# Performance work log

Measured on AMD Instinct MI355X. Metric: run time of the kernel, lower is better.

Reference implementation:

```python
import jax, jax.numpy as jnp
import numpy as np

K = 16
EPS = 1e-5
SLOPE = 0.01  # nn.LeakyReLU default


def _bn(x, g, b):
    # BatchNorm1d in training mode applied to [N, C, k] in torch == normalize
    # per-channel over (N, k) axes of [N, k, C] here. Biased variance (ddof=0).
    m = x.mean(axis=(0, 1))
    v = x.var(axis=(0, 1))
    return (x - m) * jax.lax.rsqrt(v + EPS) * g + b


def _lrelu(x):
    return jnp.where(x >= 0, x, SLOPE * x)


def setup_inputs() -> dict:
    key = jax.random.key(0)
    ks = jax.random.split(key, 24)
    N, CIN, COUT = 8192, 256, 256
    s = 0.05
    inp = {
        "fea_i": jax.random.normal(ks[0], (N, CIN), jnp.float32),
        "fea_last": jax.random.normal(ks[1], (N, CIN), jnp.float32),
        "xyz_i": jax.random.uniform(ks[2], (N, 3), jnp.float32),
        "xyz_last": jax.random.uniform(ks[3], (N, 3), jnp.float32),
        "t_i": jnp.float32(2.0),
        "t_last": jnp.float32(1.0),
        # lin_p: Linear(4,64) -> BN(64) -> LeakyReLU -> Linear(64,COUT)
        "wp1": jax.random.normal(ks[4], (4, 64), jnp.float32) * s,
        "bp1": jnp.zeros((64,), jnp.float32),
        "gp": jnp.ones((64,), jnp.float32),
        "bp": jnp.zeros((64,), jnp.float32),
        "wp2": jax.random.normal(ks[5], (64, COUT), jnp.float32) * s,
        "bp2": jnp.zeros((COUT,), jnp.float32),
        # lin_q / lin_k / lin_v
        "wq": jax.random.normal(ks[6], (CIN, COUT), jnp.float32) * s,
        "bq": jnp.zeros((COUT,), jnp.float32),
        "wk": jax.random.normal(ks[7], (CIN, COUT), jnp.float32) * s,
        "bk": jnp.zeros((COUT,), jnp.float32),
        "wv": jax.random.normal(ks[8], (CIN, COUT), jnp.float32) * s,
        "bv": jnp.zeros((COUT,), jnp.float32),
        # lin_w: BN -> LeakyReLU -> Linear(COUT,COUT) -> BN -> LeakyReLU
        "gw1": jnp.ones((COUT,), jnp.float32),
        "bw1": jnp.zeros((COUT,), jnp.float32),
        "ww": jax.random.normal(ks[9], (COUT, COUT), jnp.float32) * s,
        "bw": jnp.zeros((COUT,), jnp.float32),
        "gw2": jnp.ones((COUT,), jnp.float32),
        "bw2": jnp.zeros((COUT,), jnp.float32),
    }
    return inp


def reference(fea_i, fea_last, xyz_i, xyz_last, t_i, t_last,
              wp1, bp1, gp, bp, wp2, bp2,
              wq, bq, wk, bk, wv, bv,
              gw1, bw1, ww, bw, gw2, bw2):
    # k-NN: for each query point in xyz_last, K nearest points in xyz_i
    d2 = (jnp.sum(xyz_last * xyz_last, -1)[:, None]
          + jnp.sum(xyz_i * xyz_i, -1)[None, :]
          - 2.0 * xyz_last @ xyz_i.T)              # [N, N]
    idx = jax.lax.top_k(-d2, K)[1]                 # [N, K] neighbor idx into xyz_i

    fi = fea_i[idx]                                # [N, K, CIN]
    xi = xyz_i[idx]                                # [N, K, 3]
    # pe = xyzt_i - xyzt_last ; the gathered "last" side is the query point itself
    pe = jnp.concatenate([xi - xyz_last[:, None, :],
                          (t_i - t_last) * jnp.ones_like(xi[..., :1])], axis=-1)  # [N,K,4]
    pe = pe @ wp1 + bp1
    pe = _lrelu(_bn(pe, gp, bp))
    pe = pe @ wp2 + bp2                            # [N, K, COUT]

    q = fea_last @ wq + bq                         # [N, COUT], broadcast over K
    w = q[:, None, :] - (fi @ wk + bk) + pe        # [N, K, COUT]
    w = _lrelu(_bn(w, gw1, bw1))
    w = w @ ww + bw
    w = _lrelu(_bn(w, gw2, bw2))
    w = jax.nn.softmax(w, axis=1)                  # softmax over K neighbors

    v = fi @ wv + bv + pe                          # [N, K, COUT]
    return jnp.sum(w * v, axis=1)                  # [N, COUT]
```

## Files before the change

### kernel.cpp

```cpp
#include <hip/hip_runtime.h>
#include <hip/hip_bf16.h>
#include <math.h>

#define N     8192
#define KNN   16
#define NK    (N*KNN)
#define C     256
#define CH    64
#define EPS   1e-5f
#define SLOPE 0.01f
#define LISTMAX 512

typedef __hip_bfloat16 bf16;
typedef short bfrag __attribute__((ext_vector_type(8)));
typedef float ffrag __attribute__((ext_vector_type(4)));

__device__ __forceinline__ float b2f(bf16 x){ return __bfloat162float(x); }
__device__ __forceinline__ bf16  f2b(float x){ return __float2bfloat16(x); }
__device__ __forceinline__ float b2fu(unsigned short s){
    return __uint_as_float(((unsigned)s) << 16);
}
__device__ __forceinline__ unsigned short f2bu(float x){
    union { bf16 h; unsigned short s; } u; u.h = f2b(x); return u.s;
}

union BF8 { unsigned short s[8]; uint4 u; };

template<typename T> __device__ __forceinline__ float ldv(const void* p, int i);
template<> __device__ __forceinline__ float ldv<float>(const void* p, int i){
    return ((const float*)p)[i];
}
template<> __device__ __forceinline__ float ldv<bf16>(const void* p, int i){
    return __bfloat162float(((const bf16*)p)[i]);
}
__device__ __forceinline__ bool is_f32(const void* ti){
    return ((const unsigned short*)ti)[0] == 0;
}

template<typename T>
__device__ __forceinline__ void stage8(const void* src, size_t off,
                                       unsigned short* dst){
    if (sizeof(T) == 4){
        const float4* s = (const float4*)((const float*)src + off);
        float4 a = s[0], b = s[1];
        BF8 o;
        o.s[0]=f2bu(a.x); o.s[1]=f2bu(a.y); o.s[2]=f2bu(a.z); o.s[3]=f2bu(a.w);
        o.s[4]=f2bu(b.x); o.s[5]=f2bu(b.y); o.s[6]=f2bu(b.z); o.s[7]=f2bu(b.w);
        *(uint4*)dst = o.u;
    } else {
        *(uint4*)dst = *(const uint4*)((const unsigned short*)src + off);
    }
}

__device__ __forceinline__ int mbcnt64(unsigned long long b){
    return __builtin_amdgcn_mbcnt_hi((unsigned)(b>>32),
           __builtin_amdgcn_mbcnt_lo((unsigned)b, 0));
}
__device__ __forceinline__ unsigned d2key(float d2){
    unsigned u = __float_as_uint(d2);
    return u ^ (((unsigned)(((int)u) >> 31)) | 0x80000000u);
}

__device__ __align__(256) int    g_idx[NK];
__device__ __align__(256) float  g_S[4096];
__device__ __align__(256) float  g_Rep[4*64*256];
__device__ __align__(256) float  g_M2[2048*9];
__device__ __align__(256) float4 g_pts[N];
__device__ __align__(256) float4 g_qlast[N];
__device__ __align__(256) int    g_cellCnt[4096];
__device__ __align__(256) int    g_cellStart[4100];
__device__ __align__(256) int    g_cellCur[4096];
__device__ __align__(256) float4 g_spts[N];
__device__ __align__(256) int    g_sidx[N];
__device__ __align__(256) unsigned short g_qT [C*C];
__device__ __align__(256) unsigned short g_kT [C*C];
__device__ __align__(256) unsigned short g_vT [C*C];
__device__ __align__(256) unsigned short g_wwT[C*C];
__device__ __align__(256) unsigned short g_p2T[C*CH];
__device__ __align__(256) unsigned short g_q  [N*C];
__device__ __align__(256) unsigned short g_fkb[N*C];
__device__ __align__(256) unsigned short g_fvb[N*C];
__device__ __align__(256) bf16   g_w1[NK*C];
__device__ __align__(256) bf16   g_vv[NK*C];
__device__ __align__(256) bf16   g_w2[NK*C];

__device__ __forceinline__ int cell_of(float4 c){
    int cx = (int)(c.x*16.f); cx = cx<0?0:(cx>15?15:cx);
    int cy = (int)(c.y*16.f); cy = cy<0?0:(cy>15?15:cy);
    int cz = (int)(c.z*16.f); cz = cz<0?0:(cz>15?15:cz);
    return (cz<<8) | (cy<<4) | cx;
}

__global__ __launch_bounds__(256) void kprepall(const void* xyz_i,
        const void* xyz_last,
        const void* wq, const void* wk, const void* wv, const void* ww,
        const void* wp2, const void* ti_){
#pragma clang fp contract(off)
    const int b = blockIdx.x, tid = threadIdx.x;
    const bool f = is_f32(ti_);
    if (b < 64){
        int i = b*256 + tid;
        #pragma unroll
        for (int k = 0; k < 4; k++) g_Rep[i*4 + k] = 0.f;
        if (b < 16) g_S[i] = 0.f;
        else if (b < 32) g_cellCnt[(b-16)*256 + tid] = 0;
    } else if (b < 96){
        int p = (b-64)*256 + tid;
        float x = f ? ldv<float>(xyz_i, p*3+0) : ldv<bf16>(xyz_i, p*3+0);
        float y = f ? ldv<float>(xyz_i, p*3+1) : ldv<bf16>(xyz_i, p*3+1);
        float z = f ? ldv<float>(xyz_i, p*3+2) : ldv<bf16>(xyz_i, p*3+2);
        g_pts[p] = make_float4(x, y, z, (x*x + y*y) + z*z);
    } else if (b < 128){
        int p = (b-96)*256 + tid;
        float x = f ? ldv<float>(xyz_last, p*3+0) : ldv<bf16>(xyz_last, p*3+0);
        float y = f ? ldv<float>(xyz_last, p*3+1) : ldv<bf16>(xyz_last, p*3+1);
        float z = f ? ldv<float>(xyz_last, p*3+2) : ldv<bf16>(xyz_last, p*3+2);
        g_qlast[p] = make_float4(x, y, z, 0.f);
    } else {
        const void* src; unsigned short* dst; int K; int i0;
        if      (b <  384){ src=wq;  dst=g_qT;  K=256; i0=(b- 128)*256; }
        else if (b <  640){ src=wk;  dst=g_kT;  K=256; i0=(b- 384)*256; }
        else if (b <  896){ src=wv;  dst=g_vT;  K=256; i0=(b- 640)*256; }
        else if (b < 1152){ src=ww;  dst=g_wwT; K=256; i0=(b- 896)*256; }
        else              { src=wp2; dst=g_p2T; K=64;  i0=(b-1152)*256; }
        int i = i0 + tid;
        int k = i >> 8, n = i & 255;
        float v = f ? ldv<float>(src, i) : ldv<bf16>(src, i);
        dst[n*K + k] = f2bu(v);
    }
}

__global__ __launch_bounds__(256) void khist(){
    int p = blockIdx.x*256 + threadIdx.x;
    atomicAdd(&g_cellCnt[cell_of(g_pts[p])], 1);
}
__global__ __launch_bounds__(256) void kscan(){
    __shared__ int sc[256];
    const int tid = threadIdx.x;
    int carry = 0;
    for (int ch = 0; ch < 16; ch++){
        int i = ch*256 + tid;
        int v = g_cellCnt[i];
        sc[tid] = v;
        __syncthreads();
        for (int s = 1; s < 256; s <<= 1){
            int t_ = (tid >= s) ? sc[tid - s] : 0;
            __syncthreads();
            sc[tid] += t_;
            __syncthreads();
        }
        int excl = carry + sc[tid] - v;
        g_cellStart[i] = excl;
        g_cellCur[i]   = excl;
        carry += sc[255];
        __syncthreads();
    }
    if (tid == 0) g_cellStart[4096] = carry;
}
__global__ __launch_bounds__(256) void kscatter(){
    int p = blockIdx.x*256 + threadIdx.x;
    float4 c = g_pts[p];
    int pos = atomicAdd(&g_cellCur[cell_of(c)], 1);
    g_spts[pos] = c;
    g_sidx[pos] = p;
}

template<int D>
__device__ unsigned sel16(float qx, float qy, float qz, float sq, int lane){
#pragma clang fp contract(off)
    unsigned kk[D];
    #pragma unroll
    for (int i = 0; i < D; i++) kk[i] = 0xFFFFFFFFu;
    for (int t = 0; t < N/64; t++){
        float4 c = g_pts[t*64 + lane];
        float dot = (qx*c.x + qy*c.y) + qz*c.z;
        float d2  = (sq + c.w) - 2.0f*dot;
        unsigned u = d2key(d2);
        #pragma unroll
        for (int j = D-1; j > 0; --j){
            unsigned hi = (kk[j-1] > u) ? kk[j-1] : u;
            kk[j] = (kk[j] < hi) ? kk[j] : hi;
        }
        kk[0] = (kk[0] < u) ? kk[0] : u;
    }
    unsigned v16 = 0;
    for (int it = 0; it < 16; ++it){
        unsigned m = kk[0];
        #pragma unroll
        for (int s = 1; s < 64; s <<= 1){
            unsigned o = (unsigned)__shfl_xor((int)m, s, 64);
            m = (m < o) ? m : o;
        }
        unsigned long long ball = __ballot(kk[0] == m);
        int w = __ffsll(ball) - 1;
        if (lane == w){
            #pragma unroll
            for (int j = 0; j < D-1; j++) kk[j] = kk[j+1];
            kk[D-1] = 0xFFFFFFFFu;
        }
        v16 = m;
    }
    return v16;
}

__device__ int2 scan16(float qx, float qy, float qz, float sq, unsigned v16,
                       int lane, int* sure, int* tie){
#pragma clang fp contract(off)
    int nsure = 0, ntie = 0;
    for (int t = 0; t < N/64; t++){
        const int p = t*64 + lane;
        float4 c = g_pts[p];
        float dot = (qx*c.x + qy*c.y) + qz*c.z;
        float d2  = (sq + c.w) - 2.0f*dot;
        unsigned u = d2key(d2);
        bool bs = (u < v16), bt = (u == v16);
        unsigned long long Bs = __ballot(bs);
        unsigned long long Bt = __ballot(bt);
        if (bs){
            int pos = nsure + mbcnt64(Bs);
            if (pos < 16) sure[pos] = p;
        }
        if (bt){
            int pos = ntie + mbcnt64(Bt);
            if (pos < 16) tie[pos] = p;
        }
        nsure += (int)__popcll(Bs);
        ntie  += (int)__popcll(Bt);
    }
    return make_int2(nsure, ntie);
}

template<typename T>
__device__ void kknn_body(const void* xyz_last, int* sureL, int* tieL,
                          int* listL, float* momL){
#pragma clang fp contract(off)
    const int lane  = threadIdx.x & 63;
    const int wslot = threadIdx.x >> 6;
    const int q     = (blockIdx.x*256 + threadIdx.x) >> 6;
    const float qx = ldv<T>(xyz_last, q*3+0);
    const float qy = ldv<T>(xyz_last, q*3+1);
    const float qz = ldv<T>(xyz_last, q*3+2);
    const float sq = (qx*qx + qy*qy) + qz*qz;
    int* sure = &sureL[wslot*16];
    int* tie  = &tieL [wslot*16];
    int* list = &listL[wslot*LISTMAX];

    int cqx = (int)(qx*16.f); cqx = cqx<0?0:(cqx>15?15:cqx);
    int cqy = (int)(qy*16.f); cqy = cqy<0?0:(cqy>15?15:cqy);
    int cqz = (int)(qz*16.f); cqz = cqz<0?0:(cqz>15?15:cqz);

    int cnt0 = 0, cnt1 = 0, cs0 = 0, cs1 = 0;
    #pragma unroll
    for (int h = 0; h < 2; h++){
        int idx = lane*2 + h;
        if (idx < 125){
            int iz = idx/25, r = idx - iz*25, iy = r/5, ix = r - iy*5;
            int cx = cqx+ix-2, cy = cqy+iy-2, cz = cqz+iz-2;
            if ((unsigned)cx < 16u && (unsigned)cy < 16u && (unsigned)cz < 16u){
                int cell = (cz<<8) | (cy<<4) | cx;
                int s = g_cellStart[cell], e = g_cellStart[cell+1];
                if (h == 0){ cs0 = s; cnt0 = e - s; }
                else       { cs1 = s; cnt1 = e - s; }
            }
        }
    }
    int tot = cnt0 + cnt1;
    int incl = tot;
    #pragma unroll
    for (int s = 1; s < 64; s <<= 1){
        int u = __shfl_up(incl, s, 64);
        if (lane >= s) incl += u;
    }
    const int Tn = __shfl(incl, 63, 64);
    int base = incl - tot;
    bool full = (Tn > LISTMAX) || (Tn < 16);
    unsigned v16 = 0;
    int nsure = 0, ntie = 0;
    if (!full){
        for (int i = 0; i < cnt0; i++) list[base+i] = cs0 + i;
        for (int i = 0; i < cnt1; i++) list[base+cnt0+i] = cs1 + i;
        unsigned kk[4] = {~0u,~0u,~0u,~0u};
        int chunks = (Tn + 63) >> 6;
        for (int t = 0; t < chunks; t++){
            int li = t*64 + lane;
            unsigned u = 0xFFFFFFFFu;
            if (li < Tn){
                float4 c = g_spts[list[li]];
                float dot = (qx*c.x + qy*c.y) + qz*c.z;
                u = d2key((sq + c.w) - 2.0f*dot);
            }
            #pragma unroll
            for (int j = 3; j > 0; --j){
                unsigned hi = (kk[j-1] > u) ? kk[j-1] : u;
                kk[j] = (kk[j] < hi) ? kk[j] : hi;
            }
            kk[0] = (kk[0] < u) ? kk[0] : u;
        }
        for (int it = 0; it < 16; ++it){
            unsigned m = kk[0];
            #pragma unroll
            for (int s = 1; s < 64; s <<= 1){
                unsigned o = (unsigned)__shfl_xor((int)m, s, 64);
                m = (m < o) ? m : o;
            }
            unsigned long long ball = __ballot(kk[0] == m);
            int w = __ffsll(ball) - 1;
            if (lane == w){
                kk[0]=kk[1]; kk[1]=kk[2]; kk[2]=kk[3]; kk[3]=0xFFFFFFFFu;
            }
            v16 = m;
        }
        const float h_ = 0.0625f;
        float dmin = 1e30f;
        if (cqx-2 > 0)  dmin = fminf(dmin, qx - (float)(cqx-2)*h_);
        if (cqx+3 < 16) dmin = fminf(dmin, (float)(cqx+3)*h_ - qx);
        if (cqy-2 > 0)  dmin = fminf(dmin, qy - (float)(cqy-2)*h_);
        if (cqy+3 < 16) dmin = fminf(dmin, (float)(cqy+3)*h_ - qy);
        if (cqz-2 > 0)  dmin = fminf(dmin, qz - (float)(cqz-2)*h_);
        if (cqz+3 < 16) dmin = fminf(dmin, (float)(cqz+3)*h_ - qz);
        unsigned ub = d2key(dmin*dmin);
        if (!(v16 < ub)) full = true;
    }
    if (!full){
        int chunks = (Tn + 63) >> 6;
        for (int t = 0; t < chunks; t++){
            int li = t*64 + lane;
            unsigned u = 0xFFFFFFFFu; int oi = 0;
            if (li < Tn){
                int pos = list[li];
                float4 c = g_spts[pos];
                oi = g_sidx[pos];
                float dot = (qx*c.x + qy*c.y) + qz*c.z;
                u = d2key((sq + c.w) - 2.0f*dot);
            }
            bool bs = (li < Tn) && (u < v16);
            bool bt = (li < Tn) && (u == v16);
            unsigned long long Bs = __ballot(bs);
            unsigned long long Bt = __ballot(bt);
            if (bs){
                int pos2 = nsure + mbcnt64(Bs);
                if (pos2 < 16) sure[pos2] = oi;
            }
            if (bt){
                int pos2 = ntie + mbcnt64(Bt);
                if (pos2 < 16) tie[pos2] = oi;
            }
            nsure += (int)__popcll(Bs);
            ntie  += (int)__popcll(Bt);
        }
        if (nsure > 16 || (ntie > 16 && nsure < 16)) full = true;
    }
    const bool gridok = !full;
    if (full){
        v16 = sel16<16>(qx, qy, qz, sq, lane);
        int2 c2 = scan16(qx, qy, qz, sq, v16, lane, sure, tie);
        nsure = c2.x; ntie = c2.y;
    }
    if (nsure > 16) nsure = 16;
    int vsel = 0;
    if (lane < 16 && lane < nsure) vsel = sure[lane];
    if (gridok){
        int tv = (lane < (ntie < 16 ? ntie : 16)) ? tie[lane] : 0x7FFFFFFF;
        #pragma unroll
        for (int k = 2; k <= 16; k <<= 1)
            #pragma unroll
            for (int j = k>>1; j > 0; j >>= 1){
                int o = __shfl_xor(tv, j, 64);
                bool asc = ((lane & k) == 0);
                bool low = ((lane & j) == 0);
                int mn = tv < o ? tv : o;
                int mx = tv < o ? o : tv;
                tv = (asc == low) ? mn : mx;
            }
        int tfrom = __shfl(tv, (lane - nsure) & 63, 64);
        if (lane < 16 && lane >= nsure) vsel = tfrom;
    } else {
        if (lane < 16 && lane >= nsure) vsel = tie[lane - nsure];
    }
    float dx = 0.f, dy = 0.f, dz = 0.f;
    if (lane < 16){
        if ((unsigned)vsel >= (unsigned)N) vsel = 0;
        g_idx[q*KNN + lane] = vsel;
        float4 c = g_pts[vsel];
        dx = c.x - qx; dy = c.y - qy; dz = c.z - qz;
    }
    float mm[9] = {dx, dy, dz, dx*dx, dx*dy, dx*dz, dy*dy, dy*dz, dz*dz};
    #pragma unroll
    for (int j = 0; j < 9; j++){
        #pragma unroll
        for (int s = 1; s < 16; s <<= 1)
            mm[j] += __shfl_xor(mm[j], s, 64);
    }
    if (lane == 0){
        #pragma unroll
        for (int j = 0; j < 9; j++) momL[wslot*9 + j] = mm[j];
    }
    __syncthreads();
    if (threadIdx.x < 9){
        int t = threadIdx.x;
        g_M2[blockIdx.x*9 + t] = momL[t] + momL[9+t] + momL[18+t] + momL[27+t];
    }
}
__global__ __launch_bounds__(256) void kknn(const void* xyz_last, const void* ti_){
    __shared__ int sureL[4*16];
    __shared__ int tieL [4*16];
    __shared__ int listL[4*LISTMAX];
    __shared__ float momL[4*9];
    if (is_f32(ti_)) kknn_body<float>(xyz_last, sureL, tieL, listL, momL);
    else             kknn_body<bf16 >(xyz_last, sureL, tieL, listL, momL);
}

template<typename T>
__device__ void kgemm3m_body(const void* A, const unsigned short* BT,
                             const void* bias, unsigned short* out,
                             unsigned short* Al, unsigned short* Bl){
    const int tid  = threadIdx.x;
    const int c0   = blockIdx.x*128, r0 = blockIdx.y*128;
    const int lane = tid & 63, wv = tid >> 6;
    const int m    = lane & 15, qd = lane >> 4;
    const int rw   = (wv >> 1)*64, cw = (wv & 1)*64;
    ffrag acc[4][4];
    #pragma unroll
    for (int i = 0; i < 4; i++)
        #pragma unroll
        for (int j = 0; j < 4; j++)
            #pragma unroll
            for (int r = 0; r < 4; r++) acc[i][j][r] = 0.f;
    const int arow = tid >> 2, ach = tid & 3;
    for (int kt = 0; kt < 8; ++kt){
        __syncthreads();
        #pragma unroll
        for (int p = 0; p < 2; ++p){
            int row = arow + p*64;
            stage8<T>(A, (size_t)(r0+row)*C + kt*32 + ach*8, &Al[row*40 + ach*8]);
            *(uint4*)&Bl[row*40 + ach*8] =
                *(const uint4*)&BT[(c0+row)*C + kt*32 + ach*8];
        }
        __syncthreads();
        bfrag af[4], bfr[4];
        #pragma unroll
        for (int i = 0; i < 4; i++)
            af[i] = *(const bfrag*)&Al[(rw + i*16 + m)*40 + qd*8];
        #pragma unroll
        for (int j = 0; j < 4; j++)
            bfr[j] = *(const bfrag*)&Bl[(cw + j*16 + m)*40 + qd*8];
        #pragma unroll
        for (int i = 0; i < 4; i++)
            #pragma unroll
            for (int j = 0; j < 4; j++)
                acc[i][j] = __builtin_amdgcn_mfma_f32_16x16x32_bf16(
                                af[i], bfr[j], acc[i][j], 0, 0, 0);
    }
    float b4[4];
    #pragma unroll
    for (int j = 0; j < 4; j++) b4[j] = ldv<T>(bias, c0 + cw + j*16 + m);
    #pragma unroll
    for (int i = 0; i < 4; i++){
        #pragma unroll
        for (int r = 0; r < 4; r++){
            int row = r0 + rw + i*16 + qd*4 + r;
            unsigned short* orow = &out[(size_t)row*C];
            #pragma unroll
            for (int j = 0; j < 4; j++)
                orow[c0 + cw + j*16 + m] = f2bu(acc[i][j][r] + b4[j]);
        }
    }
}
__global__ __launch_bounds__(256) void kgemm3m(const void* fea_i, const void* fea_last,
        const void* bq, const void* bk, const void* bv, const void* ti_){
    __shared__ unsigned short Al[128*40];
    __shared__ unsigned short Bl[128*40];
    const int which = blockIdx.z;
    const void* A = (which==0) ? fea_last : fea_i;
    const unsigned short* BT = (which==0) ? g_qT : (which==1) ? g_kT : g_vT;
    const void* bias = (which==0) ? bq : (which==1) ? bk : bv;
    unsigned short* out = (which==0) ? g_q : (which==1) ? g_fkb : g_fvb;
    if (is_f32(ti_)) kgemm3m_body<float>(A, BT, bias, out, Al, Bl);
    else             kgemm3m_body<bf16 >(A, BT, bias, out, Al, Bl);
}

template<typename T>
__device__ void kfinpe_body(const void* wp1, const void* bp1,
                            const void* gp, const void* bp_,
                            const void* t_i, const void* t_last,
                            float* mTot, float* wred){
    const int tid = threadIdx.x, lane = tid & 63, wv = tid >> 6;
    float p[9];
    #pragma unroll
    for (int j = 0; j < 9; j++) p[j] = 0.f;
    for (int i = tid; i < 2048; i += 256){
        const float* m = &g_M2[i*9];
        #pragma unroll
        for (int j = 0; j < 9; j++) p[j] += m[j];
    }
    #pragma unroll
    for (int j = 0; j < 9; j++){
        #pragma unroll
        for (int s = 1; s < 64; s <<= 1) p[j] += __shfl_xor(p[j], s, 64);
    }
    if (lane == 0){
        #pragma unroll
        for (int j = 0; j < 9; j++) wred[wv*9 + j] = p[j];
    }
    __syncthreads();
    if (tid < 9) mTot[tid] = wred[tid] + wred[9+tid] + wred[18+tid] + wred[27+tid];
    __syncthreads();
    if (tid >= 64) return;
    const int c = tid;
    float M[9];
    #pragma unroll
    for (int j = 0; j < 9; j++) M[j] = mTot[j];
    const float w0 = ldv<T>(wp1, c),     w1 = ldv<T>(wp1, 64+c);
    const float w2 = ldv<T>(wp1, 128+c), w3 = ldv<T>(wp1, 192+c);
    const float dt = ldv<T>(t_i, 0) - ldv<T>(t_last, 0);
    const float be = dt*w3 + ldv<T>(bp1, c);
    const float NKf = (float)NK;
    float lin  = w0*M[0] + w1*M[1] + w2*M[2];
    float quad = w0*w0*M[3] + w1*w1*M[6] + w2*w2*M[8]
               + 2.f*(w0*w1*M[4] + w0*w2*M[5] + w1*w2*M[7]);
    float mean = (lin + NKf*be) / NKf;
    float ev2  = (quad + 2.f*be*lin + NKf*be*be) / NKf;
    float var  = ev2 - mean*mean;
    float sc   = ldv<T>(gp, c) * rsqrtf(var + EPS);
    g_S[128+c] = sc;
    g_S[192+c] = ldv<T>(bp_, c) - mean*sc;
}
__global__ void kfinpe(const void* wp1, const void* bp1, const void* gp,
                       const void* bp_, const void* t_i, const void* t_last){
    __shared__ float mTot[9];
    __shared__ float wred[4*9];
    if (is_f32(t_i)) kfinpe_body<float>(wp1, bp1, gp, bp_, t_i, t_last, mTot, wred);
    else             kfinpe_body<bf16 >(wp1, bp1, gp, bp_, t_i, t_last, mTot, wred);
}

__global__ void kfinalize(int Cn, int outOff, const void* g, const void* b,
                          const void* ti_, int repA){
    int c = threadIdx.x;
    if (c >= Cn) return;
    float s = 0.f, ss = 0.f;
    for (int r = 0; r < 64; r++){
        s  += g_Rep[((repA  )*64 + r)*256 + c];
        ss += g_Rep[((repA+1)*64 + r)*256 + c];
    }
    bool f = is_f32(ti_);
    float mean = s / (float)NK;
    float var  = ss / (float)NK - mean*mean;
    float gv = f ? ldv<float>(g, c) : ldv<bf16>(g, c);
    float bv = f ? ldv<float>(b, c) : ldv<bf16>(b, c);
    float sc = gv * rsqrtf(var + EPS);
    g_S[outOff+c]    = sc;
    g_S[outOff+Cn+c] = bv - mean*sc;
}

#define PE_LDP 132
template<typename T>
__device__ void kpe2m_body(const void* wp1, const void* bp1, const void* bp2,
                           const void* t_i, const void* t_last,
                           unsigned short* Apel, unsigned short* Bpl,
                           float* peL, int* gl, float* s1w, float* s2w){
    const int tid  = threadIdx.x;
    const int lane = tid & 63, wv = tid >> 6;
    const int m    = lane & 15, qd = lane >> 4;
    const int rw   = (wv >> 2)*64, cw = (wv & 3)*64;
    const int r0   = blockIdx.x*128;
    if (tid < 128) gl[tid] = g_idx[r0 + tid];
    { int row = tid >> 1, half = tid & 1;
      #pragma unroll
      for (int e = 0; e < 4; e++)
          *(uint4*)&Bpl[row*72 + half*32 + e*8] =
              *(const uint4*)&g_p2T[row*CH + half*32 + e*8];
    }
    __syncthreads();
    { const int kp = lane;
      const float w0 = ldv<T>(wp1, kp),     w1 = ldv<T>(wp1, 64+kp);
      const float w2 = ldv<T>(wp1, 128+kp), w3 = ldv<T>(wp1, 192+kp);
      const float b0 = ldv<T>(bp1, kp);
      const float sc = g_S[128+kp], sh = g_S[128+64+kp];
      const float dt = ldv<T>(t_i, 0) - ldv<T>(t_last, 0);
      #pragma unroll 4
      for (int p = 0; p < 16; p++){
          int row = wv*16 + p;
          int R = r0 + row; int n = R >> 4; int g = gl[row];
          float4 cp = g_pts[g];
          float4 qp = g_qlast[n];
          float dx = cp.x - qp.x;
          float dy = cp.y - qp.y;
          float dz = cp.z - qp.z;
          float v = dx*w0 + dy*w1 + dz*w2 + dt*w3 + b0;
          v = v*sc + sh;
          v = (v >= 0.f) ? v : SLOPE*v;
          Apel[row*72 + kp] = f2bu(v);
      } }
    __syncthreads();
    ffrag acc[4][4];
    #pragma unroll
    for (int i = 0; i < 4; i++)
        #pragma unroll
        for (int j = 0; j < 4; j++)
            #pragma unroll
            for (int r = 0; r < 4; r++) acc[i][j][r] = 0.f;
    #pragma unroll
    for (int ks = 0; ks < 2; ++ks){
        bfrag af[4], bfr[4];
        #pragma unroll
        for (int i = 0; i < 4; i++)
            af[i] = *(const bfrag*)&Apel[(rw + i*16 + m)*72 + ks*32 + qd*8];
        #pragma unroll
        for (int j = 0; j < 4; j++)
            bfr[j] = *(const bfrag*)&Bpl[(cw + j*16 + m)*72 + ks*32 + qd*8];
        #pragma unroll
        for (int i = 0; i < 4; i++)
            #pragma unroll
            for (int j = 0; j < 4; j++)
                acc[i][j] = __builtin_amdgcn_mfma_f32_16x16x32_bf16(
                                af[i], bfr[j], acc[i][j], 0, 0, 0);
    }
    float bp2v[4];
    #pragma unroll
    for (int j = 0; j < 4; j++) bp2v[j] = ldv<T>(bp2, cw + j*16 + m);
    #pragma unroll
    for (int i = 0; i < 4; i++)
        #pragma unroll
        for (int j = 0; j < 4; j++)
            #pragma unroll
            for (int r = 0; r < 4; r++) acc[i][j][r] += bp2v[j];

    const int rep = blockIdx.x & 63;
    const int cg  = tid & 15;
    const int rg  = tid >> 4;
    for (int h = 0; h < 2; ++h){
        __syncthreads();
        if (((wv >> 1) & 1) == h){
            int lc0 = cw & 64;
            #pragma unroll
            for (int i = 0; i < 4; i++)
                #pragma unroll
                for (int j = 0; j < 4; j++)
                    #pragma unroll
                    for (int r = 0; r < 4; r++)
                        peL[(rw + i*16 + qd*4 + r)*PE_LDP + lc0 + j*16 + m]
                            = acc[i][j][r];
        }
        __syncthreads();
        float cs8[8], cq8[8];
        #pragma unroll
        for (int e = 0; e < 8; e++){ cs8[e] = 0.f; cq8[e] = 0.f; }
        #pragma unroll
        for (int rr = 0; rr < 4; rr++){
            int row = rg*4 + rr;
            int R = r0 + row; int n = R >> 4; int g = gl[row];
            int colb = h*128 + cg*8;
            BF8 qb, kb, vb;
            qb.u = *(const uint4*)&g_q  [(size_t)n*C + colb];
            kb.u = *(const uint4*)&g_fkb[(size_t)g*C + colb];
            vb.u = *(const uint4*)&g_fvb[(size_t)g*C + colb];
            float4 p0 = *(const float4*)&peL[row*PE_LDP + cg*8];
            float4 p1 = *(const float4*)&peL[row*PE_LDP + cg*8 + 4];
            float pe8[8] = {p0.x,p0.y,p0.z,p0.w,p1.x,p1.y,p1.z,p1.w};
            BF8 w1o, vvo;
            #pragma unroll
            for (int e = 0; e < 8; e++){
                float pv = pe8[e];
                unsigned short bb = f2bu(b2fu(qb.s[e]) - b2fu(kb.s[e]) + pv);
                w1o.s[e] = bb;
                float rv = b2fu(bb);
                cs8[e] += rv; cq8[e] += rv*rv;
                vvo.s[e] = f2bu(b2fu(vb.s[e]) + pv);
            }
            *(uint4*)&((unsigned short*)g_w1)[(size_t)R*C + colb] = w1o.u;
            *(uint4*)&((unsigned short*)g_vv)[(size_t)R*C + colb] = vvo.u;
        }
        #pragma unroll
        for (int e = 0; e < 8; e++){
            cs8[e] += __shfl_xor(cs8[e], 16, 64);
            cs8[e] += __shfl_xor(cs8[e], 32, 64);
            cq8[e] += __shfl_xor(cq8[e], 16, 64);
            cq8[e] += __shfl_xor(cq8[e], 32, 64);
        }
        if (lane < 16){
            #pragma unroll
            for (int e = 0; e < 8; e++){
                s1w[wv*128 + lane*8 + e] = cs8[e];
                s2w[wv*128 + lane*8 + e] = cq8[e];
            }
        }
        __syncthreads();
        if (tid < 128){
            float a = 0.f, b = 0.f;
            #pragma unroll
            for (int w = 0; w < 8; w++){
                a += s1w[w*128 + tid];
                b += s2w[w*128 + tid];
            }
            atomicAdd(&g_Rep[(0*64 + rep)*256 + h*128 + tid], a);
            atomicAdd(&g_Rep[(1*64 + rep)*256 + h*128 + tid], b);
        }
    }
}
__global__ __launch_bounds__(512) void kpe2m(const void* wp1, const void* bp1,
        const void* bp2, const void* t_i, const void* t_last){
    __shared__ __align__(16) unsigned char smem[128*PE_LDP*4];
    __shared__ int gl[128];
    __shared__ float s1w[8*128], s2w[8*128];
    unsigned short* Apel = (unsigned short*)smem;
    unsigned short* Bpl  = Apel + 128*72;
    float* peL = (float*)smem;
    if (is_f32(t_i))
        kpe2m_body<float>(wp1, bp1, bp2, t_i, t_last, Apel, Bpl, peL,
                          gl, s1w, s2w);
    else
        kpe2m_body<bf16 >(wp1, bp1, bp2, t_i, t_last, Apel, Bpl, peL,
                          gl, s1w, s2w);
}

template<typename T>
__device__ void kgemmww_body(const void* bw, unsigned short* Al,
                             unsigned short* Bl, float* scl, float* shl,
                             float* t1w, float* t2w){
    const int tid  = threadIdx.x;
    const int c0   = blockIdx.x*128, r0 = blockIdx.y*128;
    const int lane = tid & 63, wv = tid >> 6;
    const int m    = lane & 15, qd = lane >> 4;
    const int rw   = (wv >> 1)*64, cw = (wv & 1)*64;
    scl[tid] = g_S[768 + tid]; shl[tid] = g_S[768 + C + tid];
    ffrag acc[4][4];
    #pragma unroll
    for (int i = 0; i < 4; i++)
        #pragma unroll
        for (int j = 0; j < 4; j++)
            #pragma unroll
            for (int r = 0; r < 4; r++) acc[i][j][r] = 0.f;
    const int arow = tid >> 2, ach = tid & 3;
    for (int kt = 0; kt < 8; ++kt){
        __syncthreads();
        #pragma unroll
        for (int p = 0; p < 2; ++p){
            int row = arow + p*64;
            int kk  = kt*32 + ach*8;
            BF8 in, o;
            in.u = *(const uint4*)&g_w1[(size_t)(r0+row)*C + kk];
            #pragma unroll
            for (int e = 0; e < 8; e++){
                float x = b2fu(in.s[e]);
                x = x*scl[kk+e] + shl[kk+e];
                x = (x >= 0.f) ? x : SLOPE*x;
                o.s[e] = f2bu(x);
            }
            *(uint4*)&Al[row*40 + ach*8] = o.u;
            *(uint4*)&Bl[row*40 + ach*8] =
                *(const uint4*)&g_wwT[(c0+row)*C + kt*32 + ach*8];
        }
        __syncthreads();
        bfrag af[4], bf_[4];
        #pragma unroll
        for (int i = 0; i < 4; i++)
            af[i] = *(const bfrag*)&Al[(rw + i*16 + m)*40 + qd*8];
        #pragma unroll
        for (int j = 0; j < 4; j++)
            bf_[j] = *(const bfrag*)&Bl[(cw + j*16 + m)*40 + qd*8];
        #pragma unroll
        for (int i = 0; i < 4; i++)
            #pragma unroll
            for (int j = 0; j < 4; j++)
                acc[i][j] = __builtin_amdgcn_mfma_f32_16x16x32_bf16(
                                af[i], bf_[j], acc[i][j], 0, 0, 0);
    }
    float bwv[4];
    #pragma unroll
    for (int j = 0; j < 4; j++) bwv[j] = ldv<T>(bw, c0 + cw + j*16 + m);
    float cs[4] = {0.f,0.f,0.f,0.f}, cq[4] = {0.f,0.f,0.f,0.f};
    #pragma unroll
    for (int j = 0; j < 4; j++){
        int col = c0 + cw + j*16 + m;
        #pragma unroll
        for (int i = 0; i < 4; i++){
            #pragma unroll
            for (int r = 0; r < 4; r++){
                int row = r0 + rw + i*16 + qd*4 + r;
                unsigned short bb = f2bu(acc[i][j][r] + bwv[j]);
                ((unsigned short*)g_w2)[(size_t)row*C + col] = bb;
                float rv = b2fu(bb);
                cs[j] += rv; cq[j] += rv*rv;
            }
        }
    }
    #pragma unroll
    for (int j = 0; j < 4; j++){
        cs[j] += __shfl_xor(cs[j], 16, 64); cs[j] += __shfl_xor(cs[j], 32, 64);
        cq[j] += __shfl_xor(cq[j], 16, 64); cq[j] += __shfl_xor(cq[j], 32, 64);
    }
    if (lane < 16){
        #pragma unroll
        for (int j = 0; j < 4; j++){
            t1w[(wv>>1)*128 + cw + j*16 + lane] = cs[j];
            t2w[(wv>>1)*128 + cw + j*16 + lane] = cq[j];
        }
    }
    __syncthreads();
    if (tid < 128){
        float a = t1w[tid] + t1w[128+tid];
        float b = t2w[tid] + t2w[128+tid];
        int rep = blockIdx.y & 63;
        atomicAdd(&g_Rep[(2*64 + rep)*256 + c0 + tid], a);
        atomicAdd(&g_Rep[(3*64 + rep)*256 + c0 + tid], b);
    }
}
__global__ __launch_bounds__(256) void kgemmww(const void* bw, const void* ti_){
    __shared__ unsigned short Al[128*40];
    __shared__ unsigned short Bl[128*40];
    __shared__ float scl[C], shl[C];
    __shared__ float t1w[256], t2w[256];
    if (is_f32(ti_)) kgemmww_body<float>(bw, Al, Bl, scl, shl, t1w, t2w);
    else             kgemmww_body<bf16 >(bw, Al, Bl, scl, shl, t1w, t2w);
}

__global__ __launch_bounds__(256) void kfinal(void* out, const void* ti_){
    __shared__ unsigned short w2L[16*264];
    __shared__ unsigned short vvL[16*264];
    const int n = blockIdx.x, tid = threadIdx.x;
    const unsigned short* w2g = (const unsigned short*)g_w2 + (size_t)n*KNN*C;
    const unsigned short* vvg = (const unsigned short*)g_vv + (size_t)n*KNN*C;
    #pragma unroll
    for (int p = 0; p < 2; p++){
        int off = p*2048 + tid*8;
        int row = off >> 8, col = off & 255;
        *(uint4*)&w2L[row*264 + col] = *(const uint4*)&w2g[off];
        *(uint4*)&vvL[row*264 + col] = *(const uint4*)&vvg[off];
    }
    __syncthreads();
    const int c = tid;
    const float sc = g_S[1792+c], sh = g_S[1792+C+c];
    float u[KNN];
    float m = -3.4e38f;
    #pragma unroll
    for (int k = 0; k < KNN; k++){
        float x = b2fu(w2L[k*264 + c])*sc + sh;
        x = (x >= 0.f) ? x : SLOPE*x;
        u[k] = x; m = fmaxf(m, x);
    }
    float ssum = 0.f, o = 0.f;
    #pragma unroll
    for (int k = 0; k < KNN; k++){
        float e = __expf(u[k] - m);
        ssum += e;
        o += e * b2fu(vvL[k*264 + c]);
    }
    float r = o / ssum;
    if (is_f32(ti_)) ((float*)out)[(size_t)n*C + c] = r;
    else             ((bf16*)out)[(size_t)n*C + c] = f2b(r);
}

extern "C" void kernel_launch(void* const* d_in, const int* in_sizes, int n_in,
                              void* d_out, int out_size, void* d_ws, size_t ws_size,
                              hipStream_t stream){
    const void* fea_i    = d_in[0];
    const void* fea_last = d_in[1];
    const void* xyz_i    = d_in[2];
    const void* xyz_last = d_in[3];
    const void* t_i      = d_in[4];
    const void* t_last   = d_in[5];
    const void* wp1 = d_in[6];
    const void* bp1 = d_in[7];
    const void* gp  = d_in[8];
    const void* bp_ = d_in[9];
    const void* wp2 = d_in[10];
    const void* bp2 = d_in[11];
    const void* wq  = d_in[12];
    const void* bq  = d_in[13];
    const void* wk  = d_in[14];
    const void* bk  = d_in[15];
    const void* wv  = d_in[16];
    const void* bv  = d_in[17];
    const void* gw1 = d_in[18];
    const void* bw1 = d_in[19];
    const void* ww  = d_in[20];
    const void* bw  = d_in[21];
    const void* gw2 = d_in[22];
    const void* bw2 = d_in[23];

    kprepall<<<1216, 256, 0, stream>>>(xyz_i, xyz_last, wq, wk, wv, ww, wp2, t_i);
    khist<<<32, 256, 0, stream>>>();
    kscan<<<1, 256, 0, stream>>>();
    kscatter<<<32, 256, 0, stream>>>();
    kknn<<<N/4, 256, 0, stream>>>(xyz_last, t_i);
    kgemm3m<<<dim3(2, 64, 3), 256, 0, stream>>>(fea_i, fea_last, bq, bk, bv, t_i);
    kfinpe<<<1, 256, 0, stream>>>(wp1, bp1, gp, bp_, t_i, t_last);
    kpe2m<<<dim3(NK/128), 512, 0, stream>>>(wp1, bp1, bp2, t_i, t_last);
    kfinalize<<<1, 256, 0, stream>>>(256, 768, gw1, bw1, t_i, 0);
    kgemmww<<<dim3(2, NK/128), 256, 0, stream>>>(bw, t_i);
    kfinalize<<<1, 256, 0, stream>>>(256, 1792, gw2, bw2, t_i, 2);
    kfinal<<<N, 256, 0, stream>>>(d_out, t_i);
}
```

Baseline: 325.1 us.

## Fuse histogram into prep, co-schedule kNN with QKV GEMM, split pe2m columns

The cell histogram moves into the prep kernel, and the scan kernel now resets the counts after reading them, which removes the separate khist launch and its clear. The kNN search and the three Q/K/V projection GEMMs share a single launch through block-index dispatch, so the two independent workloads run concurrently and one launch boundary disappears. The pe2m kernel goes from 512-thread full-width row tiles to 256-thread blocks split across two column halves. This shrinks shared memory per block and doubles the grid, at the cost of recomputing the per-row positional MLP front-end in both halves.

After: 319.1 us. About the same (-1.8%).

```diff
diff --git a/kernel.cpp b/kernel.cpp
--- a/kernel.cpp
+++ b/kernel.cpp
@@ -103,13 +103,14 @@
         #pragma unroll
         for (int k = 0; k < 4; k++) g_Rep[i*4 + k] = 0.f;
         if (b < 16) g_S[i] = 0.f;
-        else if (b < 32) g_cellCnt[(b-16)*256 + tid] = 0;
     } else if (b < 96){
         int p = (b-64)*256 + tid;
         float x = f ? ldv<float>(xyz_i, p*3+0) : ldv<bf16>(xyz_i, p*3+0);
         float y = f ? ldv<float>(xyz_i, p*3+1) : ldv<bf16>(xyz_i, p*3+1);
         float z = f ? ldv<float>(xyz_i, p*3+2) : ldv<bf16>(xyz_i, p*3+2);
-        g_pts[p] = make_float4(x, y, z, (x*x + y*y) + z*z);
+        float4 c = make_float4(x, y, z, (x*x + y*y) + z*z);
+        g_pts[p] = c;
+        atomicAdd(&g_cellCnt[cell_of(c)], 1);
     } else if (b < 128){
         int p = (b-96)*256 + tid;
         float x = f ? ldv<float>(xyz_last, p*3+0) : ldv<bf16>(xyz_last, p*3+0);
@@ -130,10 +131,6 @@
     }
 }
 
-__global__ __launch_bounds__(256) void khist(){
-    int p = blockIdx.x*256 + threadIdx.x;
-    atomicAdd(&g_cellCnt[cell_of(g_pts[p])], 1);
-}
 __global__ __launch_bounds__(256) void kscan(){
     __shared__ int sc[256];
     const int tid = threadIdx.x;
@@ -141,6 +138,7 @@
     for (int ch = 0; ch < 16; ch++){
         int i = ch*256 + tid;
         int v = g_cellCnt[i];
+        g_cellCnt[i] = 0;
         sc[tid] = v;
         __syncthreads();
         for (int s = 1; s < 256; s <<= 1){
@@ -231,12 +229,12 @@
 }
 
 template<typename T>
-__device__ void kknn_body(const void* xyz_last, int* sureL, int* tieL,
+__device__ void kknn_body(int bid, const void* xyz_last, int* sureL, int* tieL,
                           int* listL, float* momL){
 #pragma clang fp contract(off)
     const int lane  = threadIdx.x & 63;
     const int wslot = threadIdx.x >> 6;
-    const int q     = (blockIdx.x*256 + threadIdx.x) >> 6;
+    const int q     = (bid*256 + threadIdx.x) >> 6;
     const float qx = ldv<T>(xyz_last, q*3+0);
     const float qy = ldv<T>(xyz_last, q*3+1);
     const float qz = ldv<T>(xyz_last, q*3+2);
@@ -398,24 +396,16 @@
     __syncthreads();
     if (threadIdx.x < 9){
         int t = threadIdx.x;
-        g_M2[blockIdx.x*9 + t] = momL[t] + momL[9+t] + momL[18+t] + momL[27+t];
-    }
-}
-__global__ __launch_bounds__(256) void kknn(const void* xyz_last, const void* ti_){
-    __shared__ int sureL[4*16];
-    __shared__ int tieL [4*16];
-    __shared__ int listL[4*LISTMAX];
-    __shared__ float momL[4*9];
-    if (is_f32(ti_)) kknn_body<float>(xyz_last, sureL, tieL, listL, momL);
-    else             kknn_body<bf16 >(xyz_last, sureL, tieL, listL, momL);
+        g_M2[bid*9 + t] = momL[t] + momL[9+t] + momL[18+t] + momL[27+t];
+    }
 }
 
 template<typename T>
 __device__ void kgemm3m_body(const void* A, const unsigned short* BT,
                              const void* bias, unsigned short* out,
-                             unsigned short* Al, unsigned short* Bl){
+                             unsigned short* Al, unsigned short* Bl,
+                             int c0, int r0){
     const int tid  = threadIdx.x;
-    const int c0   = blockIdx.x*128, r0 = blockIdx.y*128;
     const int lane = tid & 63, wv = tid >> 6;
     const int m    = lane & 15, qd = lane >> 4;
     const int rw   = (wv >> 1)*64, cw = (wv & 1)*64;
@@ -466,17 +456,40 @@
         }
     }
 }
-__global__ __launch_bounds__(256) void kgemm3m(const void* fea_i, const void* fea_last,
+
+template<typename T>
+__device__ void kknngemm_body(int b, const void* xyz_last,
+        const void* fea_i, const void* fea_last,
+        const void* bq, const void* bk, const void* bv,
+        unsigned char* smem){
+    if (b < 384){
+        unsigned short* Al = (unsigned short*)smem;
+        unsigned short* Bl = Al + 128*40;
+        const int which = b >> 7, rem = b & 127;
+        const int c0 = (rem & 1)*128, r0 = (rem >> 1)*128;
+        const void* A = (which==0) ? fea_last : fea_i;
+        const unsigned short* BT = (which==0) ? g_qT : (which==1) ? g_kT : g_vT;
+        const void* bias = (which==0) ? bq : (which==1) ? bk : bv;
+        unsigned short* out = (which==0) ? g_q : (which==1) ? g_fkb : g_fvb;
+        kgemm3m_body<T>(A, BT, bias, out, Al, Bl, c0, r0);
+    } else {
+        int* base   = (int*)smem;
+        int* sureL  = base;
+        int* tieL   = base + 64;
+        int* listL  = base + 128;
+        float* momL = (float*)(base + 128 + 4*LISTMAX);
+        kknn_body<T>(b - 384, xyz_last, sureL, tieL, listL, momL);
+    }
+}
+__global__ __launch_bounds__(256) void kknngemm(const void* xyz_last,
+        const void* fea_i, const void* fea_last,
         const void* bq, const void* bk, const void* bv, const void* ti_){
-    __shared__ unsigned short Al[128*40];
-    __shared__ unsigned short Bl[128*40];
-    const int which = blockIdx.z;
-    const void* A = (which==0) ? fea_last : fea_i;
-    const unsigned short* BT = (which==0) ? g_qT : (which==1) ? g_kT : g_vT;
-    const void* bias = (which==0) ? bq : (which==1) ? bk : bv;
-    unsigned short* out = (which==0) ? g_q : (which==1) ? g_fkb : g_fvb;
-    if (is_f32(ti_)) kgemm3m_body<float>(A, BT, bias, out, Al, Bl);
-    else             kgemm3m_body<bf16 >(A, BT, bias, out, Al, Bl);
+    __shared__ __align__(16) unsigned char smem[20480];
+    const int b = blockIdx.x;
+    if (is_f32(ti_))
+        kknngemm_body<float>(b, xyz_last, fea_i, fea_last, bq, bk, bv, smem);
+    else
+        kknngemm_body<bf16 >(b, xyz_last, fea_i, fea_last, bq, bk, bv, smem);
 }
 
 template<typename T>
@@ -552,7 +565,7 @@
     g_S[outOff+Cn+c] = bv - mean*sc;
 }
 
-#define PE_LDP 132
+#define PE_LDP 68
 template<typename T>
 __device__ void kpe2m_body(const void* wp1, const void* bp1, const void* bp2,
                            const void* t_i, const void* t_last,
@@ -561,14 +574,14 @@
     const int tid  = threadIdx.x;
     const int lane = tid & 63, wv = tid >> 6;
     const int m    = lane & 15, qd = lane >> 4;
-    const int rw   = (wv >> 2)*64, cw = (wv & 3)*64;
-    const int r0   = blockIdx.x*128;
+    const int rw   = (wv >> 1)*64, cw = (wv & 1)*64;
+    const int c0   = blockIdx.x*128, r0 = blockIdx.y*128;
     if (tid < 128) gl[tid] = g_idx[r0 + tid];
     { int row = tid >> 1, half = tid & 1;
       #pragma unroll
       for (int e = 0; e < 4; e++)
           *(uint4*)&Bpl[row*72 + half*32 + e*8] =
-              *(const uint4*)&g_p2T[row*CH + half*32 + e*8];
+              *(const uint4*)&g_p2T[(c0+row)*CH + half*32 + e*8];
     }
     __syncthreads();
     { const int kp = lane;
@@ -578,8 +591,8 @@
       const float sc = g_S[128+kp], sh = g_S[128+64+kp];
       const float dt = ldv<T>(t_i, 0) - ldv<T>(t_last, 0);
       #pragma unroll 4
-      for (int p = 0; p < 16; p++){
-          int row = wv*16 + p;
+      for (int p = 0; p < 32; p++){
+          int row = wv*32 + p;
           int R = r0 + row; int n = R >> 4; int g = gl[row];
           float4 cp = g_pts[g];
           float4 qp = g_qlast[n];
@@ -617,7 +630,7 @@
     }
     float bp2v[4];
     #pragma unroll
-    for (int j = 0; j < 4; j++) bp2v[j] = ldv<T>(bp2, cw + j*16 + m);
+    for (int j = 0; j < 4; j++) bp2v[j] = ldv<T>(bp2, c0 + cw + j*16 + m);
     #pragma unroll
     for (int i = 0; i < 4; i++)
         #pragma unroll
@@ -625,20 +638,19 @@
             #pragma unroll
             for (int r = 0; r < 4; r++) acc[i][j][r] += bp2v[j];
 
-    const int rep = blockIdx.x & 63;
-    const int cg  = tid & 15;
-    const int rg  = tid >> 4;
+    const int rep = blockIdx.y & 63;
+    const int cg  = tid & 7;
+    const int rg  = tid >> 3;
     for (int h = 0; h < 2; ++h){
         __syncthreads();
-        if (((wv >> 1) & 1) == h){
-            int lc0 = cw & 64;
+        if ((wv & 1) == h){
             #pragma unroll
             for (int i = 0; i < 4; i++)
                 #pragma unroll
                 for (int j = 0; j < 4; j++)
                     #pragma unroll
                     for (int r = 0; r < 4; r++)
-                        peL[(rw + i*16 + qd*4 + r)*PE_LDP + lc0 + j*16 + m]
+                        peL[(rw + i*16 + qd*4 + r)*PE_LDP + j*16 + m]
                             = acc[i][j][r];
         }
         __syncthreads();
@@ -649,7 +661,7 @@
         for (int rr = 0; rr < 4; rr++){
             int row = rg*4 + rr;
             int R = r0 + row; int n = R >> 4; int g = gl[row];
-            int colb = h*128 + cg*8;
+            int colb = c0 + h*64 + cg*8;
             BF8 qb, kb, vb;
             qb.u = *(const uint4*)&g_q  [(size_t)n*C + colb];
             kb.u = *(const uint4*)&g_fkb[(size_t)g*C + colb];
@@ -672,36 +684,33 @@
         }
         #pragma unroll
         for (int e = 0; e < 8; e++){
-            cs8[e] += __shfl_xor(cs8[e], 16, 64);
-            cs8[e] += __shfl_xor(cs8[e], 32, 64);
-            cq8[e] += __shfl_xor(cq8[e], 16, 64);
-            cq8[e] += __shfl_xor(cq8[e], 32, 64);
-        }
-        if (lane < 16){
+            #pragma unroll
+            for (int s_ = 8; s_ < 64; s_ <<= 1){
+                cs8[e] += __shfl_xor(cs8[e], s_, 64);
+                cq8[e] += __shfl_xor(cq8[e], s_, 64);
+            }
+        }
+        if (lane < 8){
             #pragma unroll
             for (int e = 0; e < 8; e++){
-                s1w[wv*128 + lane*8 + e] = cs8[e];
-                s2w[wv*128 + lane*8 + e] = cq8[e];
+                s1w[wv*64 + lane*8 + e] = cs8[e];
+                s2w[wv*64 + lane*8 + e] = cq8[e];
             }
         }
         __syncthreads();
-        if (tid < 128){
-            float a = 0.f, b = 0.f;
-            #pragma unroll
-            for (int w = 0; w < 8; w++){
-                a += s1w[w*128 + tid];
-                b += s2w[w*128 + tid];
-            }
-            atomicAdd(&g_Rep[(0*64 + rep)*256 + h*128 + tid], a);
-            atomicAdd(&g_Rep[(1*64 + rep)*256 + h*128 + tid], b);
-        }
-    }
-}
-__global__ __launch_bounds__(512) void kpe2m(const void* wp1, const void* bp1,
+        if (tid < 64){
+            float a = s1w[tid] + s1w[64+tid] + s1w[128+tid] + s1w[192+tid];
+            float b = s2w[tid] + s2w[64+tid] + s2w[128+tid] + s2w[192+tid];
+            atomicAdd(&g_Rep[(0*64 + rep)*256 + c0 + h*64 + tid], a);
+            atomicAdd(&g_Rep[(1*64 + rep)*256 + c0 + h*64 + tid], b);
+        }
+    }
+}
+__global__ __launch_bounds__(256) void kpe2m(const void* wp1, const void* bp1,
         const void* bp2, const void* t_i, const void* t_last){
-    __shared__ __align__(16) unsigned char smem[128*PE_LDP*4];
+    __shared__ __align__(16) unsigned char smem[128*72*2*2];
     __shared__ int gl[128];
-    __shared__ float s1w[8*128], s2w[8*128];
+    __shared__ float s1w[256], s2w[256];
     unsigned short* Apel = (unsigned short*)smem;
     unsigned short* Bpl  = Apel + 128*72;
     float* peL = (float*)smem;
@@ -879,13 +888,11 @@
     const void* bw2 = d_in[23];
 
     kprepall<<<1216, 256, 0, stream>>>(xyz_i, xyz_last, wq, wk, wv, ww, wp2, t_i);
-    khist<<<32, 256, 0, stream>>>();
     kscan<<<1, 256, 0, stream>>>();
     kscatter<<<32, 256, 0, stream>>>();
-    kknn<<<N/4, 256, 0, stream>>>(xyz_last, t_i);
-    kgemm3m<<<dim3(2, 64, 3), 256, 0, stream>>>(fea_i, fea_last, bq, bk, bv, t_i);
+    kknngemm<<<2432, 256, 0, stream>>>(xyz_last, fea_i, fea_last, bq, bk, bv, t_i);
     kfinpe<<<1, 256, 0, stream>>>(wp1, bp1, gp, bp_, t_i, t_last);
-    kpe2m<<<dim3(NK/128), 512, 0, stream>>>(wp1, bp1, bp2, t_i, t_last);
+    kpe2m<<<dim3(2, NK/128), 256, 0, stream>>>(wp1, bp1, bp2, t_i, t_last);
     kfinalize<<<1, 256, 0, stream>>>(256, 768, gw1, bw1, t_i, 0);
     kgemmww<<<dim3(2, NK/128), 256, 0, stream>>>(bw, t_i);
     kfinalize<<<1, 256, 0, stream>>>(256, 1792, gw2, bw2, t_i, 2);
```
